# Performance work log

Hardware: AMD Instinct MI355X
Metric: run time of the kernel (lower is better)

## Reference

```python
import jax, jax.numpy as jnp
import numpy as np

N_NODES = 100000
F_IN = 512
HIDDEN = 64
N_CLASS = 40
N_EDGES = 3200000


def gcn_conv(x, src, dst, deg_inv_sqrt, W, b, n_nodes):
    # PyG GCNConv: linear transform, then deg^{-1/2} A_hat deg^{-1/2} aggregation, then bias
    h = x @ W  # [N, out]
    norm = deg_inv_sqrt[src] * deg_inv_sqrt[dst]  # [E+N] (includes self-loops)
    msg = h[src] * norm[:, None]  # gather + scale
    out = jax.ops.segment_sum(msg, dst, num_segments=n_nodes)  # scatter-add
    return out + b


def setup_inputs() -> dict:
    key = jax.random.key(0)
    k1, k2, k3, k4, k5 = jax.random.split(key, 5)
    x = jax.random.normal(k1, (N_NODES, F_IN), dtype=jnp.float32)
    edge_index = jax.random.randint(k2, (2, N_EDGES), 0, N_NODES, dtype=jnp.int64)
    # Glorot-style init for GCN weights
    W1 = jax.random.normal(k3, (F_IN, HIDDEN), dtype=jnp.float32) / np.sqrt(F_IN)
    b1 = jnp.zeros((HIDDEN,), dtype=jnp.float32)
    W2 = jax.random.normal(k4, (HIDDEN, N_CLASS), dtype=jnp.float32) / np.sqrt(HIDDEN)
    b2 = jnp.zeros((N_CLASS,), dtype=jnp.float32)
    return {"x": x, "edge_index": edge_index, "W1": W1, "b1": b1, "W2": W2, "b2": b2}


def reference(x, edge_index, W1, b1, W2, b2):
    n = x.shape[0]
    loops = jnp.arange(n, dtype=edge_index.dtype)
    src = jnp.concatenate([edge_index[0], loops])  # add self-loops (GCNConv default)
    dst = jnp.concatenate([edge_index[1], loops])
    deg = jax.ops.segment_sum(jnp.ones_like(dst, dtype=x.dtype), dst, num_segments=n)
    deg_inv_sqrt = jnp.where(deg > 0, jax.lax.rsqrt(deg), 0.0)
    h = gcn_conv(x, src, dst, deg_inv_sqrt, W1, b1, n)
    h = jax.nn.relu(h)  # dropout treated as eval-mode identity
    x_out = gcn_conv(h, src, dst, deg_inv_sqrt, W2, b2, n)
    return jax.nn.log_softmax(x_out, axis=1), x_out
```

## Files before the change

kernel.cpp:

```cpp
#include <hip/hip_runtime.h>
#include <math.h>

#define N_NODES 100000
#define F_IN    512
#define HIDDEN  64
#define N_CLASS 40
#define N_EDGES 3200000
#define NB      782
#define CAP     6144
#define EPB     8192
#define NPB     391

typedef int EIdx;

typedef __attribute__((ext_vector_type(8))) short short8;
typedef __attribute__((ext_vector_type(4))) float f32x4;
typedef __attribute__((ext_vector_type(4))) unsigned uint4v;

__device__ inline short f2bf(float f) {
    unsigned u = __builtin_bit_cast(unsigned, f);
    unsigned r = u + 0x7FFFu + ((u >> 16) & 1u);
    return (short)(r >> 16);
}

__device__ inline unsigned cvtpk(float lo, float hi) {
    unsigned r;
    asm("v_cvt_pk_bf16_f32 %0, %1, %2" : "=v"(r) : "v"(lo), "v"(hi));
    return r;
}

__device__ inline float bflo(unsigned w) { return __builtin_bit_cast(float, w << 16); }
__device__ inline float bfhi(unsigned w) { return __builtin_bit_cast(float, w & 0xFFFF0000u); }

__global__ __launch_bounds__(256) void wprep_kernel(const float* __restrict__ W,
                                                    short* __restrict__ Wbf,
                                                    int* __restrict__ bcur) {
    int idx = blockIdx.x * 256 + threadIdx.x;
    if (idx < NB) bcur[idx] = idx * CAP;
    int k = idx >> 6, col = idx & 63;
    Wbf[col * F_IN + (k ^ ((col & 7) << 3))] = f2bf(W[idx]);
}

__global__ __launch_bounds__(256) void part1_kernel(const EIdx* __restrict__ src,
                                                    const EIdx* __restrict__ dst,
                                                    int* __restrict__ bcur,
                                                    unsigned* __restrict__ bpacked) {
    __shared__ int hist[2 * NB];
    __shared__ int excl[NB];
    __shared__ int cur[2 * NB];
    __shared__ int delta[NB];
    __shared__ int stmp[256];
    __shared__ unsigned spk[EPB];
    __shared__ unsigned short bid[EPB];
    int t = threadIdx.x;
    int sub = t >> 7;
    int e0 = blockIdx.x * EPB;
    int dreg[32];
    for (int j = t; j < 2 * NB; j += 256) hist[j] = 0;
    __syncthreads();
#pragma unroll
    for (int k = 0; k < 32; ++k) {
        int e = e0 + k * 256 + t;
        dreg[k] = (e < N_EDGES) ? dst[e] : -1;
        if (dreg[k] >= 0) atomicAdd(&hist[sub * NB + (dreg[k] >> 7)], 1);
    }
    __syncthreads();
    {
        int i0 = 4 * t;
        int v0 = (i0 < NB) ? hist[i0] + hist[NB + i0] : 0;
        int v1 = (i0 + 1 < NB) ? hist[i0 + 1] + hist[NB + i0 + 1] : 0;
        int v2 = (i0 + 2 < NB) ? hist[i0 + 2] + hist[NB + i0 + 2] : 0;
        int v3 = (i0 + 3 < NB) ? hist[i0 + 3] + hist[NB + i0 + 3] : 0;
        int s = v0 + v1 + v2 + v3;
        stmp[t] = s;
        __syncthreads();
        for (int o = 1; o < 256; o <<= 1) {
            int a = (t >= o) ? stmp[t - o] : 0;
            __syncthreads();
            stmp[t] += a;
            __syncthreads();
        }
        int E = stmp[t] - s;
        if (i0 < NB) excl[i0] = E;
        if (i0 + 1 < NB) excl[i0 + 1] = E + v0;
        if (i0 + 2 < NB) excl[i0 + 2] = E + v0 + v1;
        if (i0 + 3 < NB) excl[i0 + 3] = E + v0 + v1 + v2;
    }
    __syncthreads();
    for (int j = t; j < NB; j += 256) {
        int h0 = hist[j], h1 = hist[NB + j];
        int tot = h0 + h1;
        int rsv = tot ? atomicAdd(&bcur[j], tot) : 0;
        delta[j] = rsv - excl[j];
        cur[j] = excl[j];
        cur[NB + j] = excl[j] + h0;
    }
    __syncthreads();
#pragma unroll
    for (int k = 0; k < 32; ++k) {
        int d = dreg[k];
        if (d >= 0) {
            int e = e0 + k * 256 + t;
            int s = src[e];
            int b = d >> 7;
            int p = atomicAdd(&cur[sub * NB + b], 1);
            spk[p] = ((unsigned)(d & 127) << 20) | (unsigned)s;
            bid[p] = (unsigned short)b;
        }
    }
    __syncthreads();
    int cnt = N_EDGES - e0;
    if (cnt > EPB) cnt = EPB;
    for (int i = t; i < cnt; i += 256) {
        int bb = bid[i];
        int pos = i + delta[bb];
        if (pos < (bb + 1) * CAP) bpacked[pos] = spk[i];
    }
}

__global__ __launch_bounds__(256) void part2_kernel(const int* __restrict__ bcur,
                                                    const unsigned* __restrict__ bpacked,
                                                    int* __restrict__ csr_src,
                                                    unsigned* __restrict__ rowmeta,
                                                    float* __restrict__ dis) {
    __shared__ unsigned ent[CAP];
    __shared__ int hist[2 * 128];
    __shared__ int stmp[128];
    __shared__ int cur[2 * 128];
    int t = threadIdx.x;
    int sub = t >> 7;
    int bk = blockIdx.x;
    int base = bk * CAP;
    int cnt = bcur[bk] - base;
    if (cnt > CAP) cnt = CAP;
    hist[t] = 0;
    __syncthreads();
    for (int i = t; i < cnt; i += 256) {
        unsigned p = bpacked[base + i];
        ent[i] = p;
        atomicAdd(&hist[sub * 128 + (p >> 20)], 1);
    }
    __syncthreads();
    if (t < 128) stmp[t] = hist[t] + hist[128 + t];
    __syncthreads();
    for (int o = 1; o < 128; o <<= 1) {
        int a = (t >= o && t < 128) ? stmp[t - o] : 0;
        __syncthreads();
        if (t < 128) stmp[t] += a;
        __syncthreads();
    }
    if (t < 128) {
        int tot = hist[t] + hist[128 + t];
        int ex = stmp[t] - tot;
        cur[t] = ex;
        cur[128 + t] = ex + hist[t];
        int n = (bk << 7) + t;
        if (n < N_NODES) {
            rowmeta[n] = (unsigned)(base + ex) | ((unsigned)tot << 23);
            dis[n] = rsqrtf((float)(tot + 1));
        }
    }
    __syncthreads();
    for (int i = t; i < cnt; i += 256) {
        unsigned p = ent[i];
        int p2 = atomicAdd(&cur[sub * 128 + (p >> 20)], 1);
        csr_src[base + p2] = (int)(p & 0xFFFFFu);
    }
}

__global__ __launch_bounds__(256) void gemm1_mfma_kernel(const float* __restrict__ x,
                                                         const short* __restrict__ Wbf,
                                                         const float* __restrict__ dis,
                                                         unsigned* __restrict__ h1b) {
    __shared__ short Wt[HIDDEN * 128];
    __shared__ short xs[128 * 72];
    int tid = threadIdx.x;
    int wave = tid >> 6, lane = tid & 63;
    int r0 = blockIdx.x * 128;
    int wr0 = r0 + wave * 32;
    int lrow = lane & 15;
    int lk = (lane >> 4) * 8;
    int bswz = (lane & 7) << 3;

    f32x4 acc[2][4];
#pragma unroll
    for (int m = 0; m < 2; ++m)
#pragma unroll
        for (int n = 0; n < 4; ++n) acc[m][n] = (f32x4)0.0f;

    int srow = tid >> 4;
    int schunk = tid & 15;
    int grow[8];
#pragma unroll
    for (int i = 0; i < 8; ++i) {
        int r = r0 + srow + i * 16;
        grow[i] = (r < N_NODES) ? r : (N_NODES - 1);
    }

    float4 xr[8];
#pragma unroll
    for (int i = 0; i < 8; ++i)
        xr[i] = *reinterpret_cast<const float4*>(x + (size_t)grow[i] * F_IN + 4 * schunk);

    const short8* Wv = (const short8*)Wbf;
    short8* Lv = (short8*)Wt;

    for (int ks = 0; ks < 8; ++ks) {
        int kg = ks * 64;
        __syncthreads();
#pragma unroll
        for (int i = 0; i < 8; ++i) {
            uint2 u = {cvtpk(xr[i].x, xr[i].y), cvtpk(xr[i].z, xr[i].w)};
            *reinterpret_cast<uint2*>(&xs[(srow + i * 16) * 72 + 4 * schunk]) = u;
        }
        if ((ks & 1) == 0) {
            int q = ks >> 1;
            for (int i = tid; i < 1024; i += 256) {
                int col = i >> 4, kc = i & 15;
                Lv[i] = Wv[col * 64 + q * 16 + kc];
            }
        }
        __syncthreads();
        if (ks < 7) {
            int kn = kg + 64;
#pragma unroll
            for (int i = 0; i < 8; ++i)
                xr[i] = *reinterpret_cast<const float4*>(x + (size_t)grow[i] * F_IN + kn + 4 * schunk);
        }
#pragma unroll
        for (int s = 0; s < 2; ++s) {
            int kwq = (ks & 1) * 64 + s * 32;
            int kloc = s * 32;
            short8 a0 = *reinterpret_cast<const short8*>(&xs[(wave * 32 + lrow) * 72 + kloc + lk]);
            short8 a1 = *reinterpret_cast<const short8*>(&xs[(wave * 32 + 16 + lrow) * 72 + kloc + lk]);
            short8 b[4];
#pragma unroll
            for (int n = 0; n < 4; ++n) {
                int c = n * 16 + lrow;
                b[n] = *reinterpret_cast<const short8*>(&Wt[c * 128 + ((kwq + lk) ^ bswz)]);
            }
#pragma unroll
            for (int n = 0; n < 4; ++n) {
                acc[0][n] = __builtin_amdgcn_mfma_f32_16x16x32_bf16(a0, b[n], acc[0][n], 0, 0, 0);
                acc[1][n] = __builtin_amdgcn_mfma_f32_16x16x32_bf16(a1, b[n], acc[1][n], 0, 0, 0);
            }
        }
    }

    int crow = (lane >> 4) * 4, ccol = lane & 15;
    bool evenc = (ccol & 1) == 0;
#pragma unroll
    for (int m = 0; m < 2; ++m) {
#pragma unroll
        for (int j = 0; j < 4; ++j) {
            int rr = wr0 + m * 16 + crow + j;
            int rs = (rr < N_NODES) ? rr : (N_NODES - 1);
            float ds = dis[rs];
            float v[4], vn[4];
#pragma unroll
            for (int n = 0; n < 4; ++n) v[n] = acc[m][n][j] * ds;
#pragma unroll
            for (int n = 0; n < 4; ++n) vn[n] = __shfl_xor(v[n], 1);
            if (rr < N_NODES && evenc) {
#pragma unroll
                for (int n = 0; n < 4; ++n)
                    h1b[(size_t)rr * 32 + ((n * 16 + ccol) >> 1)] = cvtpk(v[n], vn[n]);
            }
        }
    }
}

__global__ __launch_bounds__(256) void gather1_kernel(const unsigned* __restrict__ h1b,
                                                      const unsigned* __restrict__ rowmeta,
                                                      const int* __restrict__ csr_src,
                                                      const float* __restrict__ dis,
                                                      const float* __restrict__ b1,
                                                      float* __restrict__ out) {
    int tid = threadIdx.x;
    int n = blockIdx.x * 32 + (tid >> 3);
    int l = tid & 7;
    unsigned meta = rowmeta[n];
    int base = (int)(meta & 0x7FFFFFu);
    int deg = (int)(meta >> 23);
    const unsigned* rowp = h1b + 4 * l;
    uint4 v = *reinterpret_cast<const uint4*>(h1b + (size_t)n * 32 + 4 * l);
    float a0 = bflo(v.x), a1 = bfhi(v.x), a2 = bflo(v.y), a3 = bfhi(v.y);
    float a4 = bflo(v.z), a5 = bfhi(v.z), a6 = bflo(v.w), a7 = bfhi(v.w);
    int e = 0;
    for (; e + 3 < deg; e += 4) {
        int s0 = csr_src[base + e],     s1 = csr_src[base + e + 1];
        int s2 = csr_src[base + e + 2], s3 = csr_src[base + e + 3];
        uint4 r0 = *reinterpret_cast<const uint4*>(rowp + (size_t)s0 * 32);
        uint4 r1 = *reinterpret_cast<const uint4*>(rowp + (size_t)s1 * 32);
        uint4 r2 = *reinterpret_cast<const uint4*>(rowp + (size_t)s2 * 32);
        uint4 r3 = *reinterpret_cast<const uint4*>(rowp + (size_t)s3 * 32);
        a0 += (bflo(r0.x) + bflo(r1.x)) + (bflo(r2.x) + bflo(r3.x));
        a1 += (bfhi(r0.x) + bfhi(r1.x)) + (bfhi(r2.x) + bfhi(r3.x));
        a2 += (bflo(r0.y) + bflo(r1.y)) + (bflo(r2.y) + bflo(r3.y));
        a3 += (bfhi(r0.y) + bfhi(r1.y)) + (bfhi(r2.y) + bfhi(r3.y));
        a4 += (bflo(r0.z) + bflo(r1.z)) + (bflo(r2.z) + bflo(r3.z));
        a5 += (bfhi(r0.z) + bfhi(r1.z)) + (bfhi(r2.z) + bfhi(r3.z));
        a6 += (bflo(r0.w) + bflo(r1.w)) + (bflo(r2.w) + bflo(r3.w));
        a7 += (bfhi(r0.w) + bfhi(r1.w)) + (bfhi(r2.w) + bfhi(r3.w));
    }
    for (; e < deg; ++e) {
        int s = csr_src[base + e];
        uint4 r = *reinterpret_cast<const uint4*>(rowp + (size_t)s * 32);
        a0 += bflo(r.x); a1 += bfhi(r.x); a2 += bflo(r.y); a3 += bfhi(r.y);
        a4 += bflo(r.z); a5 += bfhi(r.z); a6 += bflo(r.w); a7 += bfhi(r.w);
    }
    float ds = dis[n];
    float4 bL = *reinterpret_cast<const float4*>(b1 + 8 * l);
    float4 bH = *reinterpret_cast<const float4*>(b1 + 8 * l + 4);
    float4 oL = {fmaxf(fmaf(a0, ds, bL.x), 0.f), fmaxf(fmaf(a1, ds, bL.y), 0.f),
                 fmaxf(fmaf(a2, ds, bL.z), 0.f), fmaxf(fmaf(a3, ds, bL.w), 0.f)};
    float4 oH = {fmaxf(fmaf(a4, ds, bH.x), 0.f), fmaxf(fmaf(a5, ds, bH.y), 0.f),
                 fmaxf(fmaf(a6, ds, bH.z), 0.f), fmaxf(fmaf(a7, ds, bH.w), 0.f)};
    float* op = out + (size_t)n * HIDDEN + 8 * l;
    *reinterpret_cast<float4*>(op) = oL;
    *reinterpret_cast<float4*>(op + 4) = oH;
}

__global__ __launch_bounds__(256) void gemm2_kernel(const float* __restrict__ x,
                                                    const float* __restrict__ W,
                                                    const float* __restrict__ dis,
                                                    unsigned* __restrict__ h2b) {
    int r = blockIdx.x * 256 + threadIdx.x;
    if (r >= N_NODES) return;
    float acc[N_CLASS];
#pragma unroll
    for (int j = 0; j < N_CLASS; ++j) acc[j] = 0.0f;
    const float* xr = x + (size_t)r * HIDDEN;
    for (int k0 = 0; k0 < HIDDEN; k0 += 4) {
        float4 xv = *reinterpret_cast<const float4*>(xr + k0);
        const float* wk = W + (size_t)k0 * N_CLASS;
#pragma unroll
        for (int j = 0; j < N_CLASS; ++j) {
            acc[j] = fmaf(xv.x, wk[j], acc[j]);
            acc[j] = fmaf(xv.y, wk[N_CLASS + j], acc[j]);
            acc[j] = fmaf(xv.z, wk[2 * N_CLASS + j], acc[j]);
            acc[j] = fmaf(xv.w, wk[3 * N_CLASS + j], acc[j]);
        }
    }
    float ds = dis[r];
    unsigned* hr = h2b + (size_t)r * 20;
#pragma unroll
    for (int q = 0; q < 5; ++q) {
        uint4v o = {cvtpk(acc[8 * q] * ds,     acc[8 * q + 1] * ds),
                    cvtpk(acc[8 * q + 2] * ds, acc[8 * q + 3] * ds),
                    cvtpk(acc[8 * q + 4] * ds, acc[8 * q + 5] * ds),
                    cvtpk(acc[8 * q + 6] * ds, acc[8 * q + 7] * ds)};
        *reinterpret_cast<uint4v*>(hr + 4 * q) = o;
    }
}

__global__ __launch_bounds__(256) void gather2_kernel(const unsigned* __restrict__ h2b,
                                                      const unsigned* __restrict__ rowmeta,
                                                      const int* __restrict__ csr_src,
                                                      const float* __restrict__ dis,
                                                      const float* __restrict__ b2,
                                                      float* __restrict__ xout,
                                                      float* __restrict__ out_ls) {
    int tid = threadIdx.x;
    int n = blockIdx.x * 32 + (tid >> 3);
    int l = tid & 7;
    bool act = l < 5;
    unsigned meta = rowmeta[n];
    int base = (int)(meta & 0x7FFFFFu);
    int deg = (int)(meta >> 23);
    const unsigned* rowp = h2b + 4 * l;
    float a0 = 0.f, a1 = 0.f, a2 = 0.f, a3 = 0.f, a4 = 0.f, a5 = 0.f, a6 = 0.f, a7 = 0.f;
    if (act) {
        uint4 v = *reinterpret_cast<const uint4*>(h2b + (size_t)n * 20 + 4 * l);
        a0 = bflo(v.x); a1 = bfhi(v.x); a2 = bflo(v.y); a3 = bfhi(v.y);
        a4 = bflo(v.z); a5 = bfhi(v.z); a6 = bflo(v.w); a7 = bfhi(v.w);
    }
    int e = 0;
    for (; e + 3 < deg; e += 4) {
        int s0 = csr_src[base + e],     s1 = csr_src[base + e + 1];
        int s2 = csr_src[base + e + 2], s3 = csr_src[base + e + 3];
        if (act) {
            uint4 r0 = *reinterpret_cast<const uint4*>(rowp + (size_t)s0 * 20);
            uint4 r1 = *reinterpret_cast<const uint4*>(rowp + (size_t)s1 * 20);
            uint4 r2 = *reinterpret_cast<const uint4*>(rowp + (size_t)s2 * 20);
            uint4 r3 = *reinterpret_cast<const uint4*>(rowp + (size_t)s3 * 20);
            a0 += (bflo(r0.x) + bflo(r1.x)) + (bflo(r2.x) + bflo(r3.x));
            a1 += (bfhi(r0.x) + bfhi(r1.x)) + (bfhi(r2.x) + bfhi(r3.x));
            a2 += (bflo(r0.y) + bflo(r1.y)) + (bflo(r2.y) + bflo(r3.y));
            a3 += (bfhi(r0.y) + bfhi(r1.y)) + (bfhi(r2.y) + bfhi(r3.y));
            a4 += (bflo(r0.z) + bflo(r1.z)) + (bflo(r2.z) + bflo(r3.z));
            a5 += (bfhi(r0.z) + bfhi(r1.z)) + (bfhi(r2.z) + bfhi(r3.z));
            a6 += (bflo(r0.w) + bflo(r1.w)) + (bflo(r2.w) + bflo(r3.w));
            a7 += (bfhi(r0.w) + bfhi(r1.w)) + (bfhi(r2.w) + bfhi(r3.w));
        }
    }
    for (; e < deg; ++e) {
        int s = csr_src[base + e];
        if (act) {
            uint4 r = *reinterpret_cast<const uint4*>(rowp + (size_t)s * 20);
            a0 += bflo(r.x); a1 += bfhi(r.x); a2 += bflo(r.y); a3 += bfhi(r.y);
            a4 += bflo(r.z); a5 += bfhi(r.z); a6 += bflo(r.w); a7 += bfhi(r.w);
        }
    }
    float ds = dis[n];
    float v0 = 0.f, v1 = 0.f, v2 = 0.f, v3 = 0.f, v4 = 0.f, v5 = 0.f, v6 = 0.f, v7 = 0.f;
    if (act) {
        float4 bL = *reinterpret_cast<const float4*>(b2 + 8 * l);
        float4 bH = *reinterpret_cast<const float4*>(b2 + 8 * l + 4);
        v0 = fmaf(a0, ds, bL.x); v1 = fmaf(a1, ds, bL.y);
        v2 = fmaf(a2, ds, bL.z); v3 = fmaf(a3, ds, bL.w);
        v4 = fmaf(a4, ds, bH.x); v5 = fmaf(a5, ds, bH.y);
        v6 = fmaf(a6, ds, bH.z); v7 = fmaf(a7, ds, bH.w);
    }
    float mx = act ? fmaxf(fmaxf(fmaxf(v0, v1), fmaxf(v2, v3)),
                           fmaxf(fmaxf(v4, v5), fmaxf(v6, v7))) : -INFINITY;
    mx = fmaxf(mx, __shfl_xor(mx, 1));
    mx = fmaxf(mx, __shfl_xor(mx, 2));
    mx = fmaxf(mx, __shfl_xor(mx, 4));
    float sum = act ? ((expf(v0 - mx) + expf(v1 - mx)) + (expf(v2 - mx) + expf(v3 - mx))) +
                      ((expf(v4 - mx) + expf(v5 - mx)) + (expf(v6 - mx) + expf(v7 - mx))) : 0.f;
    sum += __shfl_xor(sum, 1);
    sum += __shfl_xor(sum, 2);
    sum += __shfl_xor(sum, 4);
    if (act) {
        float ls = mx + logf(sum);
        float* xp = xout + (size_t)n * N_CLASS + 8 * l;
        float* lp = out_ls + (size_t)n * N_CLASS + 8 * l;
        float4 xoL = {v0, v1, v2, v3};
        float4 xoH = {v4, v5, v6, v7};
        float4 loL = {v0 - ls, v1 - ls, v2 - ls, v3 - ls};
        float4 loH = {v4 - ls, v5 - ls, v6 - ls, v7 - ls};
        *reinterpret_cast<float4*>(xp) = xoL;
        *reinterpret_cast<float4*>(xp + 4) = xoH;
        *reinterpret_cast<float4*>(lp) = loL;
        *reinterpret_cast<float4*>(lp + 4) = loH;
    }
}

extern "C" void kernel_launch(void* const* d_in, const int* in_sizes, int n_in,
                              void* d_out, int out_size, void* d_ws, size_t ws_size,
                              hipStream_t stream) {
    const float* x  = (const float*)d_in[0];
    const EIdx*  ei = (const EIdx*)d_in[1];
    const float* W1 = (const float*)d_in[2];
    const float* b1 = (const float*)d_in[3];
    const float* W2 = (const float*)d_in[4];
    const float* b2 = (const float*)d_in[5];
    const EIdx* src = ei;
    const EIdx* dst = ei + N_EDGES;

    float* out_ls = (float*)d_out;
    float* x_out  = out_ls + (size_t)N_NODES * N_CLASS;

    char* w = (char*)d_ws;
    int*      bcur    = (int*)w;       w += 1024 * 4;
    float*    dis     = (float*)w;     w += 100352 * 4;
    unsigned* rowmeta = (unsigned*)w;  w += 100352 * 4;
    short*    Wbf     = (short*)w;     w += (size_t)F_IN * HIDDEN * 2;
    unsigned* bpacked = (unsigned*)w;
    unsigned* h1b     = (unsigned*)w;  w += (size_t)NB * CAP * 4;
    int*      csr_src = (int*)w;       w += (size_t)NB * CAP * 4;
    unsigned* h2b     = (unsigned*)w;  w += (size_t)N_NODES * 20 * 4;
    float*    agg1    = (float*)w;     w += (size_t)N_NODES * HIDDEN * 4;

    const int B = 256;
    int gG  = N_NODES / 32;
    int gN  = (N_NODES + B - 1) / B;
    int gM1 = (N_NODES + 127) / 128;

    wprep_kernel<<<(F_IN * HIDDEN) / B, B, 0, stream>>>(W1, Wbf, bcur);
    part1_kernel<<<NPB, B, 0, stream>>>(src, dst, bcur, bpacked);
    part2_kernel<<<NB, B, 0, stream>>>(bcur, bpacked, csr_src, rowmeta, dis);

    gemm1_mfma_kernel<<<gM1, B, 0, stream>>>(x, Wbf, dis, h1b);
    gather1_kernel<<<gG, B, 0, stream>>>(h1b, rowmeta, csr_src, dis, b1, agg1);

    gemm2_kernel<<<gN, B, 0, stream>>>(agg1, W2, dis, h2b);
    gather2_kernel<<<gG, B, 0, stream>>>(h2b, rowmeta, csr_src, dis, b2, x_out, out_ls);
}
```

Before: 271.8 us.

## Fuse layer-1 gather with layer-2 GEMM and unroll edge gathers by eight

```diff
diff --git a/kernel.cpp b/kernel.cpp
--- a/kernel.cpp
+++ b/kernel.cpp
@@ -270,14 +270,21 @@
     }
 }
 
-__global__ __launch_bounds__(256) void gather1_kernel(const unsigned* __restrict__ h1b,
-                                                      const unsigned* __restrict__ rowmeta,
-                                                      const int* __restrict__ csr_src,
-                                                      const float* __restrict__ dis,
-                                                      const float* __restrict__ b1,
-                                                      float* __restrict__ out) {
+__global__ __launch_bounds__(256) void gather1_gemm2_kernel(const unsigned* __restrict__ h1b,
+                                                            const unsigned* __restrict__ rowmeta,
+                                                            const int* __restrict__ csr_src,
+                                                            const float* __restrict__ dis,
+                                                            const float* __restrict__ b1,
+                                                            const float* __restrict__ W2,
+                                                            unsigned* __restrict__ h2b) {
+    __shared__ float W2s[HIDDEN * N_CLASS];
+    __shared__ float aggs[32 * HIDDEN];
+    __shared__ float outs[32 * N_CLASS];
     int tid = threadIdx.x;
-    int n = blockIdx.x * 32 + (tid >> 3);
+    for (int i = tid; i < HIDDEN * N_CLASS; i += 256) W2s[i] = W2[i];
+
+    int nl = tid >> 3;
+    int n = blockIdx.x * 32 + nl;
     int l = tid & 7;
     unsigned meta = rowmeta[n];
     int base = (int)(meta & 0x7FFFFFu);
@@ -287,21 +294,35 @@
     float a0 = bflo(v.x), a1 = bfhi(v.x), a2 = bflo(v.y), a3 = bfhi(v.y);
     float a4 = bflo(v.z), a5 = bfhi(v.z), a6 = bflo(v.w), a7 = bfhi(v.w);
     int e = 0;
-    for (; e + 3 < deg; e += 4) {
+    for (; e + 7 < deg; e += 8) {
         int s0 = csr_src[base + e],     s1 = csr_src[base + e + 1];
         int s2 = csr_src[base + e + 2], s3 = csr_src[base + e + 3];
+        int s4 = csr_src[base + e + 4], s5 = csr_src[base + e + 5];
+        int s6 = csr_src[base + e + 6], s7 = csr_src[base + e + 7];
         uint4 r0 = *reinterpret_cast<const uint4*>(rowp + (size_t)s0 * 32);
         uint4 r1 = *reinterpret_cast<const uint4*>(rowp + (size_t)s1 * 32);
         uint4 r2 = *reinterpret_cast<const uint4*>(rowp + (size_t)s2 * 32);
         uint4 r3 = *reinterpret_cast<const uint4*>(rowp + (size_t)s3 * 32);
-        a0 += (bflo(r0.x) + bflo(r1.x)) + (bflo(r2.x) + bflo(r3.x));
-        a1 += (bfhi(r0.x) + bfhi(r1.x)) + (bfhi(r2.x) + bfhi(r3.x));
-        a2 += (bflo(r0.y) + bflo(r1.y)) + (bflo(r2.y) + bflo(r3.y));
-        a3 += (bfhi(r0.y) + bfhi(r1.y)) + (bfhi(r2.y) + bfhi(r3.y));
-        a4 += (bflo(r0.z) + bflo(r1.z)) + (bflo(r2.z) + bflo(r3.z));
-        a5 += (bfhi(r0.z) + bfhi(r1.z)) + (bfhi(r2.z) + bfhi(r3.z));
-        a6 += (bflo(r0.w) + bflo(r1.w)) + (bflo(r2.w) + bflo(r3.w));
-        a7 += (bfhi(r0.w) + bfhi(r1.w)) + (bfhi(r2.w) + bfhi(r3.w));
+        uint4 r4 = *reinterpret_cast<const uint4*>(rowp + (size_t)s4 * 32);
+        uint4 r5 = *reinterpret_cast<const uint4*>(rowp + (size_t)s5 * 32);
+        uint4 r6 = *reinterpret_cast<const uint4*>(rowp + (size_t)s6 * 32);
+        uint4 r7 = *reinterpret_cast<const uint4*>(rowp + (size_t)s7 * 32);
+        a0 += ((bflo(r0.x) + bflo(r1.x)) + (bflo(r2.x) + bflo(r3.x))) +
+              ((bflo(r4.x) + bflo(r5.x)) + (bflo(r6.x) + bflo(r7.x)));
+        a1 += ((bfhi(r0.x) + bfhi(r1.x)) + (bfhi(r2.x) + bfhi(r3.x))) +
+              ((bfhi(r4.x) + bfhi(r5.x)) + (bfhi(r6.x) + bfhi(r7.x)));
+        a2 += ((bflo(r0.y) + bflo(r1.y)) + (bflo(r2.y) + bflo(r3.y))) +
+              ((bflo(r4.y) + bflo(r5.y)) + (bflo(r6.y) + bflo(r7.y)));
+        a3 += ((bfhi(r0.y) + bfhi(r1.y)) + (bfhi(r2.y) + bfhi(r3.y))) +
+              ((bfhi(r4.y) + bfhi(r5.y)) + (bfhi(r6.y) + bfhi(r7.y)));
+        a4 += ((bflo(r0.z) + bflo(r1.z)) + (bflo(r2.z) + bflo(r3.z))) +
+              ((bflo(r4.z) + bflo(r5.z)) + (bflo(r6.z) + bflo(r7.z)));
+        a5 += ((bfhi(r0.z) + bfhi(r1.z)) + (bfhi(r2.z) + bfhi(r3.z))) +
+              ((bfhi(r4.z) + bfhi(r5.z)) + (bfhi(r6.z) + bfhi(r7.z)));
+        a6 += ((bflo(r0.w) + bflo(r1.w)) + (bflo(r2.w) + bflo(r3.w))) +
+              ((bflo(r4.w) + bflo(r5.w)) + (bflo(r6.w) + bflo(r7.w)));
+        a7 += ((bfhi(r0.w) + bfhi(r1.w)) + (bfhi(r2.w) + bfhi(r3.w))) +
+              ((bfhi(r4.w) + bfhi(r5.w)) + (bfhi(r6.w) + bfhi(r7.w)));
     }
     for (; e < deg; ++e) {
         int s = csr_src[base + e];
@@ -310,47 +331,40 @@
         a4 += bflo(r.z); a5 += bfhi(r.z); a6 += bflo(r.w); a7 += bfhi(r.w);
     }
     float ds = dis[n];
-    float4 bL = *reinterpret_cast<const float4*>(b1 + 8 * l);
-    float4 bH = *reinterpret_cast<const float4*>(b1 + 8 * l + 4);
-    float4 oL = {fmaxf(fmaf(a0, ds, bL.x), 0.f), fmaxf(fmaf(a1, ds, bL.y), 0.f),
-                 fmaxf(fmaf(a2, ds, bL.z), 0.f), fmaxf(fmaf(a3, ds, bL.w), 0.f)};
-    float4 oH = {fmaxf(fmaf(a4, ds, bH.x), 0.f), fmaxf(fmaf(a5, ds, bH.y), 0.f),
-                 fmaxf(fmaf(a6, ds, bH.z), 0.f), fmaxf(fmaf(a7, ds, bH.w), 0.f)};
-    float* op = out + (size_t)n * HIDDEN + 8 * l;
-    *reinterpret_cast<float4*>(op) = oL;
-    *reinterpret_cast<float4*>(op + 4) = oH;
-}
-
-__global__ __launch_bounds__(256) void gemm2_kernel(const float* __restrict__ x,
-                                                    const float* __restrict__ W,
-                                                    const float* __restrict__ dis,
-                                                    unsigned* __restrict__ h2b) {
-    int r = blockIdx.x * 256 + threadIdx.x;
-    if (r >= N_NODES) return;
-    float acc[N_CLASS];
-#pragma unroll
-    for (int j = 0; j < N_CLASS; ++j) acc[j] = 0.0f;
-    const float* xr = x + (size_t)r * HIDDEN;
-    for (int k0 = 0; k0 < HIDDEN; k0 += 4) {
-        float4 xv = *reinterpret_cast<const float4*>(xr + k0);
-        const float* wk = W + (size_t)k0 * N_CLASS;
-#pragma unroll
-        for (int j = 0; j < N_CLASS; ++j) {
-            acc[j] = fmaf(xv.x, wk[j], acc[j]);
-            acc[j] = fmaf(xv.y, wk[N_CLASS + j], acc[j]);
-            acc[j] = fmaf(xv.z, wk[2 * N_CLASS + j], acc[j]);
-            acc[j] = fmaf(xv.w, wk[3 * N_CLASS + j], acc[j]);
-        }
-    }
-    float ds = dis[r];
-    unsigned* hr = h2b + (size_t)r * 20;
-#pragma unroll
-    for (int q = 0; q < 5; ++q) {
-        uint4v o = {cvtpk(acc[8 * q] * ds,     acc[8 * q + 1] * ds),
-                    cvtpk(acc[8 * q + 2] * ds, acc[8 * q + 3] * ds),
-                    cvtpk(acc[8 * q + 4] * ds, acc[8 * q + 5] * ds),
-                    cvtpk(acc[8 * q + 6] * ds, acc[8 * q + 7] * ds)};
-        *reinterpret_cast<uint4v*>(hr + 4 * q) = o;
+    {
+        float4 bL = *reinterpret_cast<const float4*>(b1 + 8 * l);
+        float4 bH = *reinterpret_cast<const float4*>(b1 + 8 * l + 4);
+        float4 oL = {fmaxf(fmaf(a0, ds, bL.x), 0.f), fmaxf(fmaf(a1, ds, bL.y), 0.f),
+                     fmaxf(fmaf(a2, ds, bL.z), 0.f), fmaxf(fmaf(a3, ds, bL.w), 0.f)};
+        float4 oH = {fmaxf(fmaf(a4, ds, bH.x), 0.f), fmaxf(fmaf(a5, ds, bH.y), 0.f),
+                     fmaxf(fmaf(a6, ds, bH.z), 0.f), fmaxf(fmaf(a7, ds, bH.w), 0.f)};
+        float* ap = aggs + nl * HIDDEN + 8 * l;
+        *reinterpret_cast<float4*>(ap) = oL;
+        *reinterpret_cast<float4*>(ap + 4) = oH;
+    }
+    __syncthreads();
+    {
+        float o0 = 0.f, o1 = 0.f, o2 = 0.f, o3 = 0.f, o4 = 0.f;
+        const float* ar = aggs + nl * HIDDEN;
+        int c0 = 5 * l;
+#pragma unroll 8
+        for (int k = 0; k < HIDDEN; ++k) {
+            float av = ar[k];
+            const float* wr = W2s + k * N_CLASS + c0;
+            o0 = fmaf(av, wr[0], o0);
+            o1 = fmaf(av, wr[1], o1);
+            o2 = fmaf(av, wr[2], o2);
+            o3 = fmaf(av, wr[3], o3);
+            o4 = fmaf(av, wr[4], o4);
+        }
+        float* op = outs + nl * N_CLASS + c0;
+        op[0] = o0 * ds; op[1] = o1 * ds; op[2] = o2 * ds; op[3] = o3 * ds; op[4] = o4 * ds;
+    }
+    __syncthreads();
+    for (int i = tid; i < 32 * 20; i += 256) {
+        int n3 = i / 20, c3 = i % 20;
+        const float* op = outs + n3 * N_CLASS + 2 * c3;
+        h2b[(size_t)(blockIdx.x * 32 + n3) * 20 + c3] = cvtpk(op[0], op[1]);
     }
 }
 
@@ -376,22 +390,36 @@
         a4 = bflo(v.z); a5 = bfhi(v.z); a6 = bflo(v.w); a7 = bfhi(v.w);
     }
     int e = 0;
-    for (; e + 3 < deg; e += 4) {
+    for (; e + 7 < deg; e += 8) {
         int s0 = csr_src[base + e],     s1 = csr_src[base + e + 1];
         int s2 = csr_src[base + e + 2], s3 = csr_src[base + e + 3];
+        int s4 = csr_src[base + e + 4], s5 = csr_src[base + e + 5];
+        int s6 = csr_src[base + e + 6], s7 = csr_src[base + e + 7];
         if (act) {
             uint4 r0 = *reinterpret_cast<const uint4*>(rowp + (size_t)s0 * 20);
             uint4 r1 = *reinterpret_cast<const uint4*>(rowp + (size_t)s1 * 20);
             uint4 r2 = *reinterpret_cast<const uint4*>(rowp + (size_t)s2 * 20);
             uint4 r3 = *reinterpret_cast<const uint4*>(rowp + (size_t)s3 * 20);
-            a0 += (bflo(r0.x) + bflo(r1.x)) + (bflo(r2.x) + bflo(r3.x));
-            a1 += (bfhi(r0.x) + bfhi(r1.x)) + (bfhi(r2.x) + bfhi(r3.x));
-            a2 += (bflo(r0.y) + bflo(r1.y)) + (bflo(r2.y) + bflo(r3.y));
-            a3 += (bfhi(r0.y) + bfhi(r1.y)) + (bfhi(r2.y) + bfhi(r3.y));
-            a4 += (bflo(r0.z) + bflo(r1.z)) + (bflo(r2.z) + bflo(r3.z));
-            a5 += (bfhi(r0.z) + bfhi(r1.z)) + (bfhi(r2.z) + bfhi(r3.z));
-            a6 += (bflo(r0.w) + bflo(r1.w)) + (bflo(r2.w) + bflo(r3.w));
-            a7 += (bfhi(r0.w) + bfhi(r1.w)) + (bfhi(r2.w) + bfhi(r3.w));
+            uint4 r4 = *reinterpret_cast<const uint4*>(rowp + (size_t)s4 * 20);
+            uint4 r5 = *reinterpret_cast<const uint4*>(rowp + (size_t)s5 * 20);
+            uint4 r6 = *reinterpret_cast<const uint4*>(rowp + (size_t)s6 * 20);
+            uint4 r7 = *reinterpret_cast<const uint4*>(rowp + (size_t)s7 * 20);
+            a0 += ((bflo(r0.x) + bflo(r1.x)) + (bflo(r2.x) + bflo(r3.x))) +
+                  ((bflo(r4.x) + bflo(r5.x)) + (bflo(r6.x) + bflo(r7.x)));
+            a1 += ((bfhi(r0.x) + bfhi(r1.x)) + (bfhi(r2.x) + bfhi(r3.x))) +
+                  ((bfhi(r4.x) + bfhi(r5.x)) + (bfhi(r6.x) + bfhi(r7.x)));
+            a2 += ((bflo(r0.y) + bflo(r1.y)) + (bflo(r2.y) + bflo(r3.y))) +
+                  ((bflo(r4.y) + bflo(r5.y)) + (bflo(r6.y) + bflo(r7.y)));
+            a3 += ((bfhi(r0.y) + bfhi(r1.y)) + (bfhi(r2.y) + bfhi(r3.y))) +
+                  ((bfhi(r4.y) + bfhi(r5.y)) + (bfhi(r6.y) + bfhi(r7.y)));
+            a4 += ((bflo(r0.z) + bflo(r1.z)) + (bflo(r2.z) + bflo(r3.z))) +
+                  ((bflo(r4.z) + bflo(r5.z)) + (bflo(r6.z) + bflo(r7.z)));
+            a5 += ((bfhi(r0.z) + bfhi(r1.z)) + (bfhi(r2.z) + bfhi(r3.z))) +
+                  ((bfhi(r4.z) + bfhi(r5.z)) + (bfhi(r6.z) + bfhi(r7.z)));
+            a6 += ((bflo(r0.w) + bflo(r1.w)) + (bflo(r2.w) + bflo(r3.w))) +
+                  ((bflo(r4.w) + bflo(r5.w)) + (bflo(r6.w) + bflo(r7.w)));
+            a7 += ((bfhi(r0.w) + bfhi(r1.w)) + (bfhi(r2.w) + bfhi(r3.w))) +
+                  ((bfhi(r4.w) + bfhi(r5.w)) + (bfhi(r6.w) + bfhi(r7.w)));
         }
     }
     for (; e < deg; ++e) {
@@ -461,11 +489,9 @@
     unsigned* h1b     = (unsigned*)w;  w += (size_t)NB * CAP * 4;
     int*      csr_src = (int*)w;       w += (size_t)NB * CAP * 4;
     unsigned* h2b     = (unsigned*)w;  w += (size_t)N_NODES * 20 * 4;
-    float*    agg1    = (float*)w;     w += (size_t)N_NODES * HIDDEN * 4;
 
     const int B = 256;
     int gG  = N_NODES / 32;
-    int gN  = (N_NODES + B - 1) / B;
     int gM1 = (N_NODES + 127) / 128;
 
     wprep_kernel<<<(F_IN * HIDDEN) / B, B, 0, stream>>>(W1, Wbf, bcur);
@@ -473,8 +499,7 @@
     part2_kernel<<<NB, B, 0, stream>>>(bcur, bpacked, csr_src, rowmeta, dis);
 
     gemm1_mfma_kernel<<<gM1, B, 0, stream>>>(x, Wbf, dis, h1b);
-    gather1_kernel<<<gG, B, 0, stream>>>(h1b, rowmeta, csr_src, dis, b1, agg1);
-
-    gemm2_kernel<<<gN, B, 0, stream>>>(agg1, W2, dis, h2b);
+    gather1_gemm2_kernel<<<gG, B, 0, stream>>>(h1b, rowmeta, csr_src, dis, b1, W2, h2b);
+
     gather2_kernel<<<gG, B, 0, stream>>>(h2b, rowmeta, csr_src, dis, b2, x_out, out_ls);
 }
```

Measured after the change: 263.4 us. 3.1% less time.
